# Performance work log

Measured on AMD Instinct MI355X. Metric: run time of the kernel, lower is better.

The kernel has to match this reference:

```python
import jax, jax.numpy as jnp
import numpy as np

N_SAMPLE, N_ATOMS, N_TOKENS, N_CHAINS = 4, 8192, 1024, 8
AF3_THR = 1.1  # af3_clash_threshold
COUNT_THR = 100  # total_clash > 100
REL_THR = 0.5    # relative_clash > 0.5


def setup_inputs() -> dict:
    key = jax.random.key(0)
    k1, = jax.random.split(key, 1)
    # coords spread out a bit so clashes are sparse-ish but nonzero
    pred_coordinate = jax.random.normal(k1, (N_SAMPLE, N_ATOMS, 3), dtype=jnp.float32) * 5.0
    # balanced sorted chain assignment per token: guarantees all ids 0..N_CHAINS-1 present
    asym_id = ((jnp.arange(N_TOKENS) * N_CHAINS) // N_TOKENS).astype(jnp.int32)
    # monotone atoms -> tokens map (N_ATOMS // N_TOKENS atoms per token)
    atom_to_token_idx = (jnp.arange(N_ATOMS) // (N_ATOMS // N_TOKENS)).astype(jnp.int32)
    return {
        "pred_coordinate": pred_coordinate,
        "asym_id": asym_id,
        "atom_to_token_idx": atom_to_token_idx,
    }


def reference(pred_coordinate, asym_id, atom_to_token_idx):
    # Per-atom chain id, then one-hot chain membership M: [N_atoms, N_chains]
    atom_chain = asym_id[atom_to_token_idx]
    M = jax.nn.one_hot(atom_chain, N_CHAINS, dtype=pred_coordinate.dtype)
    n_per_chain = M.sum(axis=0)  # [C] atoms per chain

    # Squared pairwise distances via gram expansion (avoids [S,N,N,3] diff tensor)
    sq = jnp.sum(pred_coordinate * pred_coordinate, axis=-1)          # [S, N]
    gram = jnp.einsum('snd,smd->snm', pred_coordinate, pred_coordinate)  # [S, N, N]
    d2 = sq[:, :, None] + sq[:, None, :] - 2.0 * gram                 # [S, N, N]

    # dist < thr  <=>  d2 < thr^2 (both non-negative)
    clash = (d2 < AF3_THR * AF3_THR).astype(pred_coordinate.dtype)

    # counts[s, a, b] = #{(i in chain a, j in chain b) : clash}; two small GEMMs
    counts = jnp.einsum('snm,na,mb->sab', clash, M, M)  # [S, C, C]

    # original only fills strict off-diagonal pairs (i < j, mirrored); diagonal stays 0
    off = 1.0 - jnp.eye(N_CHAINS, dtype=counts.dtype)
    total = counts * off
    min_n = jnp.minimum(n_per_chain[:, None], n_per_chain[None, :])
    rel = total / min_n

    af3_clash_details = jnp.stack([total, rel], axis=-1)  # [S, C, C, 2]
    has_af3_clash = (total > COUNT_THR) | (rel > REL_THR)  # [S, C, C] bool
    return has_af3_clash, af3_clash_details
```

## Files before the change

### kernel.cpp

```cpp
#include <hip/hip_runtime.h>

#define NS 4
#define NA 8192
#define NTOK 1024
#define NC 8
#define THREADS 256
#define JSLOTS 4
#define JPB (THREADS * JSLOTS)
#define TI 64
#define TPJ (JPB / TI)
#define GRIDX 448


__global__ __launch_bounds__(THREADS)
void setup_kernel(const float* __restrict__ coords, const int* __restrict__ asym,
                  const int* __restrict__ a2t, float4* __restrict__ staged,
                  int* __restrict__ chain, int* __restrict__ counts) {
  const float THR2 = 1.21f;
  int idx = blockIdx.x * THREADS + threadIdx.x;
  float x = coords[3 * idx + 0], y = coords[3 * idx + 1], z = coords[3 * idx + 2];
  staged[idx] = make_float4(2.0f * x, 2.0f * y, 2.0f * z,
                            2.0f * (THR2 - (x * x + y * y + z * z)));
  if (idx < NA) chain[idx] = asym[a2t[idx]];
  if (idx < NS * NC * NC) counts[idx] = 0;
}

__global__ __launch_bounds__(THREADS, 8)
void clash_kernel(const float4* __restrict__ staged, const int* __restrict__ chain,
                  int* __restrict__ counts) {
  __shared__ int red[NC * NC];

  const int tid = threadIdx.x;
  const int s = blockIdx.z;

  int f = blockIdx.x, jb = 1;
  while (f >= 8 * jb * (jb + 1)) ++jb;
  const int ib = f - 8 * jb * (jb - 1);

  if (tid < NC * NC) red[tid] = 0;

  const float4* __restrict__ sb = staged + (size_t)s * NA;
  const float TWO_THR2 = 2.42f;

  float xj[JSLOTS], yj[JSLOTS], zj[JSLOTS], tj2[JSLOTS];
  int bj[JSLOTS];
#pragma unroll
  for (int u = 0; u < JSLOTS; ++u) {
    int j = jb * JPB + u * THREADS + tid;
    float4 cj = sb[j];
    xj[u] = cj.x; yj[u] = cj.y; zj[u] = cj.z;
    tj2[u] = TWO_THR2 - cj.w;
    bj[u] = chain[j];
  }

  int myi = chain[ib * TI + (tid & 63)];
  const int A = __builtin_amdgcn_readfirstlane(myi);
  bool uniform = __all(myi == A);

  int b0[JSLOTS];
#pragma unroll
  for (int u = 0; u < JSLOTS; ++u) {
    b0[u] = __builtin_amdgcn_readfirstlane(bj[u]);
    uniform = uniform && __all(bj[u] == b0[u]);
  }

  __syncthreads();

  const float4* __restrict__ tg = sb + ib * TI;

  if (uniform) {
    int acc[JSLOTS] = {0, 0, 0, 0};
#pragma unroll 8
    for (int t = 0; t < TI; ++t) {
      float4 ci = tg[t];
#pragma unroll
      for (int u = 0; u < JSLOTS; ++u) {
        float d = fmaf(ci.x, xj[u], fmaf(ci.y, yj[u], fmaf(ci.z, zj[u], ci.w)));
        acc[u] += __popcll(__ballot(d > tj2[u]));
      }
    }
    if ((tid & 63) == 0) {
#pragma unroll
      for (int u = 0; u < JSLOTS; ++u) {
        if (acc[u]) {
          atomicAdd(&red[A * NC + b0[u]], acc[u]);
          atomicAdd(&red[b0[u] * NC + A], acc[u]);
        }
      }
    }
  } else {
    for (int t = 0; t < TI; ++t) {
      float4 ci = tg[t];
      int a = chain[ib * TI + t];
#pragma unroll
      for (int u = 0; u < JSLOTS; ++u) {
        float d = fmaf(ci.x, xj[u], fmaf(ci.y, yj[u], fmaf(ci.z, zj[u], ci.w)));
        if (d > tj2[u]) {
          atomicAdd(&red[a * NC + bj[u]], 1);
          atomicAdd(&red[bj[u] * NC + a], 1);
        }
      }
    }
  }

  __syncthreads();
  if (tid < NC * NC) {
    int v = red[tid];
    if (v) atomicAdd(&counts[s * NC * NC + tid], v);
  }
}

__global__ __launch_bounds__(THREADS)
void finalize_kernel(const int* __restrict__ asym, const int* __restrict__ counts,
                     float* __restrict__ out) {
  __shared__ int hist[NC];
  int tid = threadIdx.x;
  if (tid < NC) hist[tid] = 0;
  __syncthreads();
  for (int t = tid; t < NTOK; t += THREADS) atomicAdd(&hist[asym[t]], NA / NTOK);
  __syncthreads();

  int c = counts[tid];
  int a = (tid >> 3) & 7, b = tid & 7;
  float total = (a == b) ? 0.0f : (float)c;
  float minn = (float)min(hist[a], hist[b]);
  float rel = total / minn;
  out[tid] = ((total > 100.0f) || (rel > 0.5f)) ? 1.0f : 0.0f;
  out[256 + 2 * tid + 0] = total;
  out[256 + 2 * tid + 1] = rel;
}

extern "C" void kernel_launch(void* const* d_in, const int* in_sizes, int n_in,
                              void* d_out, int out_size, void* d_ws, size_t ws_size,
                              hipStream_t stream) {
  const float* coords = (const float*)d_in[0];
  const int* asym = (const int*)d_in[1];
  const int* a2t = (const int*)d_in[2];
  float* out = (float*)d_out;

  float4* staged = (float4*)d_ws;
  int* chain = (int*)(staged + NS * NA);
  int* counts = chain + NA;

  setup_kernel<<<dim3(NS * NA / THREADS), THREADS, 0, stream>>>(coords, asym, a2t,
                                                                staged, chain, counts);
  clash_kernel<<<dim3(GRIDX, 1, NS), THREADS, 0, stream>>>(staged, chain, counts);
  finalize_kernel<<<1, THREADS, 0, stream>>>(asym, counts, out);
}
```

Baseline: 77.75 us.

## Switch staged coords to SoA and use packed FMA with mixed ballot/VALU counting

Splits the staged float4 array into separate X/Y/Z/W arrays so the inner loop can load pairs of i-atoms as 2-wide vectors. It uses packed two-lane FMAs (v_pk_fma_f32 on CDNA) to evaluate two i-atoms per instruction. Half the j-slots still count through ballot+popcount, while the other half count per-lane with plain adds and are reduced once at the end with shuffles. The aim is to cut FMA issue count and spread the counting work between the scalar and vector pipes, at the cost of more registers and four separate loads per pair.

```diff
diff --git a/kernel.cpp b/kernel.cpp
--- a/kernel.cpp
+++ b/kernel.cpp
@@ -8,26 +8,30 @@
 #define JSLOTS 4
 #define JPB (THREADS * JSLOTS)
 #define TI 64
-#define TPJ (JPB / TI)
 #define GRIDX 448
+
+typedef float v2f __attribute__((ext_vector_type(2)));
 
 
 __global__ __launch_bounds__(THREADS)
 void setup_kernel(const float* __restrict__ coords, const int* __restrict__ asym,
-                  const int* __restrict__ a2t, float4* __restrict__ staged,
-                  int* __restrict__ chain, int* __restrict__ counts) {
+                  const int* __restrict__ a2t, float* __restrict__ X,
+                  float* __restrict__ Y, float* __restrict__ Z,
+                  float* __restrict__ W, int* __restrict__ chain,
+                  int* __restrict__ counts) {
   const float THR2 = 1.21f;
   int idx = blockIdx.x * THREADS + threadIdx.x;
   float x = coords[3 * idx + 0], y = coords[3 * idx + 1], z = coords[3 * idx + 2];
-  staged[idx] = make_float4(2.0f * x, 2.0f * y, 2.0f * z,
-                            2.0f * (THR2 - (x * x + y * y + z * z)));
+  X[idx] = 2.0f * x; Y[idx] = 2.0f * y; Z[idx] = 2.0f * z;
+  W[idx] = 2.0f * (THR2 - (x * x + y * y + z * z));
   if (idx < NA) chain[idx] = asym[a2t[idx]];
   if (idx < NS * NC * NC) counts[idx] = 0;
 }
 
 __global__ __launch_bounds__(THREADS, 8)
-void clash_kernel(const float4* __restrict__ staged, const int* __restrict__ chain,
-                  int* __restrict__ counts) {
+void clash_kernel(const float* __restrict__ X, const float* __restrict__ Y,
+                  const float* __restrict__ Z, const float* __restrict__ W,
+                  const int* __restrict__ chain, int* __restrict__ counts) {
   __shared__ int red[NC * NC];
 
   const int tid = threadIdx.x;
@@ -39,17 +43,18 @@
 
   if (tid < NC * NC) red[tid] = 0;
 
-  const float4* __restrict__ sb = staged + (size_t)s * NA;
+  const int base = s * NA;
   const float TWO_THR2 = 2.42f;
 
-  float xj[JSLOTS], yj[JSLOTS], zj[JSLOTS], tj2[JSLOTS];
+  v2f xjd[JSLOTS], yjd[JSLOTS], zjd[JSLOTS];
+  float tj2[JSLOTS];
   int bj[JSLOTS];
 #pragma unroll
   for (int u = 0; u < JSLOTS; ++u) {
     int j = jb * JPB + u * THREADS + tid;
-    float4 cj = sb[j];
-    xj[u] = cj.x; yj[u] = cj.y; zj[u] = cj.z;
-    tj2[u] = TWO_THR2 - cj.w;
+    float xx = X[base + j], yy = Y[base + j], zz = Z[base + j], ww = W[base + j];
+    xjd[u] = (v2f){xx, xx}; yjd[u] = (v2f){yy, yy}; zjd[u] = (v2f){zz, zz};
+    tj2[u] = TWO_THR2 - ww;
     bj[u] = chain[j];
   }
 
@@ -66,20 +71,42 @@
 
   __syncthreads();
 
-  const float4* __restrict__ tg = sb + ib * TI;
+  const v2f* __restrict__ Xp = (const v2f*)(X + base + ib * TI);
+  const v2f* __restrict__ Yp = (const v2f*)(Y + base + ib * TI);
+  const v2f* __restrict__ Zp = (const v2f*)(Z + base + ib * TI);
+  const v2f* __restrict__ Wp = (const v2f*)(W + base + ib * TI);
 
   if (uniform) {
-    int acc[JSLOTS] = {0, 0, 0, 0};
+    int accS0 = 0, accS1 = 0, accV2 = 0, accV3 = 0;
 #pragma unroll 8
-    for (int t = 0; t < TI; ++t) {
-      float4 ci = tg[t];
+    for (int p = 0; p < TI / 2; ++p) {
+      v2f cx = Xp[p], cy = Yp[p], cz = Zp[p], cw = Wp[p];
+      v2f d0 = __builtin_elementwise_fma(cx, xjd[0],
+               __builtin_elementwise_fma(cy, yjd[0],
+               __builtin_elementwise_fma(cz, zjd[0], cw)));
+      v2f d1 = __builtin_elementwise_fma(cx, xjd[1],
+               __builtin_elementwise_fma(cy, yjd[1],
+               __builtin_elementwise_fma(cz, zjd[1], cw)));
+      v2f d2 = __builtin_elementwise_fma(cx, xjd[2],
+               __builtin_elementwise_fma(cy, yjd[2],
+               __builtin_elementwise_fma(cz, zjd[2], cw)));
+      v2f d3 = __builtin_elementwise_fma(cx, xjd[3],
+               __builtin_elementwise_fma(cy, yjd[3],
+               __builtin_elementwise_fma(cz, zjd[3], cw)));
+      accS0 += __popcll(__ballot(d0.x > tj2[0]));
+      accS0 += __popcll(__ballot(d0.y > tj2[0]));
+      accS1 += __popcll(__ballot(d1.x > tj2[1]));
+      accS1 += __popcll(__ballot(d1.y > tj2[1]));
+      accV2 += (d2.x > tj2[2]) + (d2.y > tj2[2]);
+      accV3 += (d3.x > tj2[3]) + (d3.y > tj2[3]);
+    }
 #pragma unroll
-      for (int u = 0; u < JSLOTS; ++u) {
-        float d = fmaf(ci.x, xj[u], fmaf(ci.y, yj[u], fmaf(ci.z, zj[u], ci.w)));
-        acc[u] += __popcll(__ballot(d > tj2[u]));
-      }
+    for (int m = 32; m >= 1; m >>= 1) {
+      accV2 += __shfl_xor(accV2, m, 64);
+      accV3 += __shfl_xor(accV3, m, 64);
     }
     if ((tid & 63) == 0) {
+      int acc[JSLOTS] = {accS0, accS1, accV2, accV3};
 #pragma unroll
       for (int u = 0; u < JSLOTS; ++u) {
         if (acc[u]) {
@@ -90,11 +117,12 @@
     }
   } else {
     for (int t = 0; t < TI; ++t) {
-      float4 ci = tg[t];
+      float cx = X[base + ib * TI + t], cy = Y[base + ib * TI + t];
+      float cz = Z[base + ib * TI + t], cw = W[base + ib * TI + t];
       int a = chain[ib * TI + t];
 #pragma unroll
       for (int u = 0; u < JSLOTS; ++u) {
-        float d = fmaf(ci.x, xj[u], fmaf(ci.y, yj[u], fmaf(ci.z, zj[u], ci.w)));
+        float d = fmaf(cx, xjd[u].x, fmaf(cy, yjd[u].x, fmaf(cz, zjd[u].x, cw)));
         if (d > tj2[u]) {
           atomicAdd(&red[a * NC + bj[u]], 1);
           atomicAdd(&red[bj[u] * NC + a], 1);
@@ -138,12 +166,16 @@
   const int* a2t = (const int*)d_in[2];
   float* out = (float*)d_out;
 
-  float4* staged = (float4*)d_ws;
-  int* chain = (int*)(staged + NS * NA);
+  float* X = (float*)d_ws;
+  float* Y = X + NS * NA;
+  float* Z = Y + NS * NA;
+  float* W = Z + NS * NA;
+  int* chain = (int*)(W + NS * NA);
   int* counts = chain + NA;
 
   setup_kernel<<<dim3(NS * NA / THREADS), THREADS, 0, stream>>>(coords, asym, a2t,
-                                                                staged, chain, counts);
-  clash_kernel<<<dim3(GRIDX, 1, NS), THREADS, 0, stream>>>(staged, chain, counts);
+                                                                X, Y, Z, W, chain,
+                                                                counts);
+  clash_kernel<<<dim3(GRIDX, 1, NS), THREADS, 0, stream>>>(X, Y, Z, W, chain, counts);
   finalize_kernel<<<1, THREADS, 0, stream>>>(asym, counts, out);
 }
```

After: 87.10 us. 1.12x slower.
